# Kernel optimization log

Measured on AMD Instinct MI355X. Metric: run time of the kernel, lower is better.

Reference implementation:

```python
import jax, jax.numpy as jnp
import numpy as np

B = 4096      # batch of states
N = 32        # SVGD particles per state
D_ACT = 16    # action dim
D_OBS = 64    # obs dim
H = 256       # critic hidden width
STEPS = 3     # num_svgd_steps
LR = 0.1      # svgd_lr
LIMIT = 1.0   # act_limit


def q_mlp(obs, x, w1, b1, w2, b2, w3, b3):
    # SAC-style critic: q(obs, a) -> scalar per row. obs/x: [BN, *]
    h = jnp.concatenate([obs, x], axis=-1)
    h = jax.nn.relu(h @ w1 + b1)
    h = jax.nn.relu(h @ w2 + b2)
    return (h @ w3 + b3)[..., 0]  # [BN]


def rbf_kernel(X, Y):
    # X: [B, N, D] (differentiable), Y: [B, N, D] (detached copy of X)
    diff = X[:, :, None, :] - Y[:, None, :, :]          # [B, N, N, D]
    dist_sq = jnp.sum(diff * diff, axis=-1)             # [B, N, N]
    # median heuristic bandwidth per batch element
    med = jnp.median(dist_sq.reshape(dist_sq.shape[0], -1), axis=-1)
    h = med / np.log(N) + 1e-8
    gamma = jax.lax.stop_gradient(1.0 / (2.0 * h))      # [B]
    K = jnp.exp(-gamma[:, None, None] * dist_sq)        # [B, N, N]
    # dK/dX (grad wrt first argument)
    K_grad = -2.0 * gamma[:, None, None, None] * diff * K[..., None]  # [B,N,N,D]
    return K, diff, gamma, K_grad


def setup_inputs() -> dict:
    key = jax.random.key(0)
    ks = jax.random.split(key, 6)
    BN = B * N
    sc = lambda k, shp: jax.random.normal(k, shp, jnp.float32) * 0.05
    return {
        "obs": jax.random.normal(ks[0], (BN, D_OBS), jnp.float32),
        "a": jax.random.normal(ks[1], (BN, D_ACT), jnp.float32),
        "w1": sc(ks[2], (D_OBS + D_ACT, H)),
        "b1": jnp.zeros((H,), jnp.float32),
        "w2": sc(ks[3], (H, H)),
        "b2": jnp.zeros((H,), jnp.float32),
        "w3": sc(ks[4], (H, 1)),
        "b3": jnp.zeros((1,), jnp.float32),
    }


def reference(obs, a, w1, b1, w2, b2, w3, b3):
    # a0 arrives detached in the original (sampler(obs, a0.detach(), ...))
    a = jax.lax.stop_gradient(a)
    logp = jnp.zeros((B, N), jnp.float32)
    q_fn = lambda X: q_mlp(obs, X, w1, b1, w2, b2, w3, b3)
    q_vals = None
    for _ in range(STEPS):
        # log_prob = min(q1, q1) == q1; score = d(sum q)/dX via vjp
        q_vals, vjp_fn = jax.vjp(q_fn, a)                 # q_vals: [BN]
        score, = vjp_fn(jnp.ones_like(q_vals))            # [BN, D_ACT]
        X = a.reshape(B, N, D_ACT)
        S = score.reshape(B, N, D_ACT)
        K, diff, gamma, K_grad = rbf_kernel(X, jax.lax.stop_gradient(X))
        # phi = (K.detach() @ score - K_grad.sum(2)) / N
        drive = jnp.einsum('bij,bjd->bid', jax.lax.stop_gradient(K), S)
        phi = (drive - K_grad.sum(axis=2)) / N            # [B, N, D]
        # logp correction terms
        tmp1 = (K_grad * S[:, None, :, :]).sum(-1).mean(-1)                 # [B, N]
        tmp2 = -2.0 * gamma[:, None] * (((-K_grad) * diff).sum(-1)
                                        - D_ACT * K).mean(-1)               # [B, N]
        logp = logp - LR * (tmp1 + tmp2)
        # svgd_optim + clamp + detach
        a = a + LR * phi.reshape(B * N, D_ACT)
        a = jax.lax.stop_gradient(jnp.clip(a, -LIMIT, LIMIT))
    return a.reshape(B, N, D_ACT), logp, q_vals
```

## Files before the change

kernel.cpp:

```cpp
#include <hip/hip_runtime.h>
#include <hip/hip_bf16.h>
#include <math.h>

#define BNROWS (4096*32)
#define RB     64
#define LN32   3.4657359027997265f

typedef __attribute__((ext_vector_type(8))) short bf16x8;
typedef __attribute__((ext_vector_type(4))) float f32x4;

static __device__ __forceinline__ ushort f2bf(float x) {
    union { __hip_bfloat16 h; ushort u; } cv;
    cv.h = __float2bfloat16(x);
    return cv.u;
}

__global__ void obs_to_bf16(const float* __restrict__ obs,
                            ushort* __restrict__ obs_bf) {
    size_t i = ((size_t)blockIdx.x * 256 + threadIdx.x) * 4;
    float4 v = *(const float4*)&obs[i];
    ushort4 o;
    o.x = f2bf(v.x); o.y = f2bf(v.y); o.z = f2bf(v.z); o.w = f2bf(v.w);
    *(ushort4*)&obs_bf[i] = o;
}

__global__ void prep_pack(const float* __restrict__ w1,
                          const float* __restrict__ w2,
                          ushort* __restrict__ pB1, ushort* __restrict__ pB2,
                          ushort* __restrict__ pB3, ushort* __restrict__ pB4) {
    int g = blockIdx.x * 256 + threadIdx.x;
    ushort out[8];
    ushort* dst;
    if (g < 3072) {
        int lane = g & 63, gc = g >> 6;
        int t = gc / 3, c = gc % 3;
        int m = lane & 15, q = lane >> 4, n = t * 16 + m;
        #pragma unroll
        for (int j = 0; j < 8; ++j) {
            int k = c * 32 + q * 8 + j;
            out[j] = f2bf((k < 80) ? w1[k * 256 + n] : 0.f);
        }
        dst = &pB1[g * 8];
    } else if (g < 11264) {
        int gg = g - 3072;
        int lane = gg & 63, gc = gg >> 6;
        int t = gc >> 3, c = gc & 7;
        int m = lane & 15, q = lane >> 4, n = t * 16 + m;
        #pragma unroll
        for (int j = 0; j < 8; ++j)
            out[j] = f2bf(w2[(c * 32 + q * 8 + j) * 256 + n]);
        dst = &pB2[gg * 8];
    } else if (g < 19456) {
        int gg = g - 11264;
        int lane = gg & 63, gc = gg >> 6;
        int t = gc >> 3, c = gc & 7;
        int m = lane & 15, q = lane >> 4;
        #pragma unroll
        for (int j = 0; j < 8; ++j)
            out[j] = f2bf(w2[(t * 16 + m) * 256 + c * 32 + q * 8 + j]);
        dst = &pB3[gg * 8];
    } else if (g < 19968) {
        int gg = g - 19456;
        int lane = gg & 63, c = gg >> 6;
        int m = lane & 15, q = lane >> 4;
        #pragma unroll
        for (int j = 0; j < 8; ++j)
            out[j] = f2bf(w1[(64 + m) * 256 + c * 32 + q * 8 + j]);
        dst = &pB4[gg * 8];
    } else return;
    *(uint4*)dst = *(uint4*)out;
}

__global__ __launch_bounds__(512) void mlp_mfma(
    const ushort* __restrict__ obs_bf,
    const float* __restrict__ a_in,
    const float* __restrict__ b1,
    const float* __restrict__ b2,
    const float* __restrict__ w3,
    const float* __restrict__ b3,
    const ushort* __restrict__ pB1, const ushort* __restrict__ pB2,
    const ushort* __restrict__ pB3, const ushort* __restrict__ pB4,
    float* __restrict__ score,
    float* __restrict__ qout)
{
    __shared__ __align__(16) ushort B0[RB * 264];
    __shared__ __align__(16) ushort B1s[RB * 104];
    __shared__ float qpart[8][RB];
    __shared__ float bias1[256], bias2[256], w3s[256];

    const int tid  = threadIdx.x;
    const int row0 = blockIdx.x * RB;

    {
        int r = tid >> 3, ch = tid & 7;
        *(uint4*)&B1s[r * 104 + ch * 8] =
            *(const uint4*)&obs_bf[(size_t)(row0 + r) * 64 + ch * 8];
    }
    if (tid < 256) {
        int r = tid >> 2, d0 = (tid & 3) * 4;
        float4 av = *(const float4*)&a_in[(size_t)(row0 + r) * 16 + d0];
        ushort4 pv;
        pv.x = f2bf(av.x); pv.y = f2bf(av.y); pv.z = f2bf(av.z); pv.w = f2bf(av.w);
        *(ushort4*)&B1s[r * 104 + 64 + d0] = pv;
        ushort4 zv; zv.x = zv.y = zv.z = zv.w = 0;
        *(ushort4*)&B1s[r * 104 + 80 + d0] = zv;
        bias1[tid] = b1[tid]; bias2[tid] = b2[tid]; w3s[tid] = w3[tid];
    }
    __syncthreads();

    const int lane = tid & 63;
    const int w    = tid >> 6;
    const int m    = lane & 15;
    const int q    = lane >> 4;
    const int qk   = q * 8;

    f32x4 acc[4][2];
    unsigned relumask = 0u;

    #pragma unroll
    for (int tc = 0; tc < 2; ++tc)
        #pragma unroll
        for (int rt = 0; rt < 4; ++rt) acc[rt][tc] = (f32x4){0.f, 0.f, 0.f, 0.f};
    for (int c = 0; c < 3; ++c) {
        bf16x8 af[4];
        #pragma unroll
        for (int rt = 0; rt < 4; ++rt)
            af[rt] = *(const bf16x8*)&B1s[(rt * 16 + m) * 104 + c * 32 + qk];
        #pragma unroll
        for (int tc = 0; tc < 2; ++tc) {
            bf16x8 wfr = *(const bf16x8*)&pB1[(((w * 2 + tc) * 3 + c) * 64 + lane) * 8];
            #pragma unroll
            for (int rt = 0; rt < 4; ++rt)
                acc[rt][tc] = __builtin_amdgcn_mfma_f32_16x16x32_bf16(wfr, af[rt], acc[rt][tc], 0, 0, 0);
        }
    }
    #pragma unroll
    for (int tc = 0; tc < 2; ++tc) {
        const float4 bv = *(const float4*)&bias1[(w * 2 + tc) * 16 + q * 4];
        const float bva[4] = {bv.x, bv.y, bv.z, bv.w};
        #pragma unroll
        for (int rt = 0; rt < 4; ++rt) {
            ushort4 pk;
            float z0 = acc[rt][tc][0] + bva[0];
            float z1 = acc[rt][tc][1] + bva[1];
            float z2 = acc[rt][tc][2] + bva[2];
            float z3 = acc[rt][tc][3] + bva[3];
            if (z0 > 0.f) relumask |= 1u << (rt * 8 + tc * 4 + 0);
            if (z1 > 0.f) relumask |= 1u << (rt * 8 + tc * 4 + 1);
            if (z2 > 0.f) relumask |= 1u << (rt * 8 + tc * 4 + 2);
            if (z3 > 0.f) relumask |= 1u << (rt * 8 + tc * 4 + 3);
            pk.x = f2bf(fmaxf(z0, 0.f)); pk.y = f2bf(fmaxf(z1, 0.f));
            pk.z = f2bf(fmaxf(z2, 0.f)); pk.w = f2bf(fmaxf(z3, 0.f));
            *(ushort4*)&B0[(rt * 16 + m) * 264 + (w * 2 + tc) * 16 + q * 4] = pk;
        }
    }
    __syncthreads();

    #pragma unroll
    for (int tc = 0; tc < 2; ++tc)
        #pragma unroll
        for (int rt = 0; rt < 4; ++rt) acc[rt][tc] = (f32x4){0.f, 0.f, 0.f, 0.f};
    for (int c = 0; c < 8; ++c) {
        bf16x8 af[4];
        #pragma unroll
        for (int rt = 0; rt < 4; ++rt)
            af[rt] = *(const bf16x8*)&B0[(rt * 16 + m) * 264 + c * 32 + qk];
        #pragma unroll
        for (int tc = 0; tc < 2; ++tc) {
            bf16x8 wfr = *(const bf16x8*)&pB2[(((w * 2 + tc) * 8 + c) * 64 + lane) * 8];
            #pragma unroll
            for (int rt = 0; rt < 4; ++rt)
                acc[rt][tc] = __builtin_amdgcn_mfma_f32_16x16x32_bf16(wfr, af[rt], acc[rt][tc], 0, 0, 0);
        }
    }
    __syncthreads();
    {
        float qp[4] = {0.f, 0.f, 0.f, 0.f};
        #pragma unroll
        for (int tc = 0; tc < 2; ++tc) {
            const float4 bv = *(const float4*)&bias2[(w * 2 + tc) * 16 + q * 4];
            const float4 wv = *(const float4*)&w3s[(w * 2 + tc) * 16 + q * 4];
            const float bva[4] = {bv.x, bv.y, bv.z, bv.w};
            const float wva[4] = {wv.x, wv.y, wv.z, wv.w};
            #pragma unroll
            for (int rt = 0; rt < 4; ++rt) {
                ushort4 pk; float dz[4];
                #pragma unroll
                for (int i = 0; i < 4; ++i) {
                    float z = acc[rt][tc][i] + bva[i];
                    if (z > 0.f) { qp[rt] += z * wva[i]; dz[i] = wva[i]; }
                    else         { dz[i] = 0.f; }
                }
                pk.x = f2bf(dz[0]); pk.y = f2bf(dz[1]);
                pk.z = f2bf(dz[2]); pk.w = f2bf(dz[3]);
                *(ushort4*)&B0[(rt * 16 + m) * 264 + (w * 2 + tc) * 16 + q * 4] = pk;
            }
        }
        #pragma unroll
        for (int rt = 0; rt < 4; ++rt) {
            float v = qp[rt];
            v += __shfl_xor(v, 16); v += __shfl_xor(v, 32);
            if (q == 0) qpart[w][rt * 16 + m] = v;
        }
    }
    __syncthreads();

    if (tid < RB) {
        float qs = b3[0];
        #pragma unroll
        for (int ww = 0; ww < 8; ++ww) qs += qpart[ww][tid];
        qout[row0 + tid] = qs;
    }

    #pragma unroll
    for (int tc = 0; tc < 2; ++tc)
        #pragma unroll
        for (int rt = 0; rt < 4; ++rt) acc[rt][tc] = (f32x4){0.f, 0.f, 0.f, 0.f};
    for (int c = 0; c < 8; ++c) {
        bf16x8 af[4];
        #pragma unroll
        for (int rt = 0; rt < 4; ++rt)
            af[rt] = *(const bf16x8*)&B0[(rt * 16 + m) * 264 + c * 32 + qk];
        #pragma unroll
        for (int tc = 0; tc < 2; ++tc) {
            bf16x8 wfr = *(const bf16x8*)&pB3[(((w * 2 + tc) * 8 + c) * 64 + lane) * 8];
            #pragma unroll
            for (int rt = 0; rt < 4; ++rt)
                acc[rt][tc] = __builtin_amdgcn_mfma_f32_16x16x32_bf16(wfr, af[rt], acc[rt][tc], 0, 0, 0);
        }
    }
    __syncthreads();
    #pragma unroll
    for (int rt = 0; rt < 4; ++rt)
        #pragma unroll
        for (int tc = 0; tc < 2; ++tc) {
            ushort4 pk;
            pk.x = f2bf((relumask >> (rt * 8 + tc * 4 + 0)) & 1u ? acc[rt][tc][0] : 0.f);
            pk.y = f2bf((relumask >> (rt * 8 + tc * 4 + 1)) & 1u ? acc[rt][tc][1] : 0.f);
            pk.z = f2bf((relumask >> (rt * 8 + tc * 4 + 2)) & 1u ? acc[rt][tc][2] : 0.f);
            pk.w = f2bf((relumask >> (rt * 8 + tc * 4 + 3)) & 1u ? acc[rt][tc][3] : 0.f);
            *(ushort4*)&B0[(rt * 16 + m) * 264 + (w * 2 + tc) * 16 + q * 4] = pk;
        }
    __syncthreads();

    if (w < 4) {
        f32x4 acc2 = (f32x4){0.f, 0.f, 0.f, 0.f};
        for (int c = 0; c < 8; ++c) {
            bf16x8 af = *(const bf16x8*)&B0[(w * 16 + m) * 264 + c * 32 + qk];
            bf16x8 wfr = *(const bf16x8*)&pB4[(c * 64 + lane) * 8];
            acc2 = __builtin_amdgcn_mfma_f32_16x16x32_bf16(wfr, af, acc2, 0, 0, 0);
        }
        float4 o; o.x = acc2[0]; o.y = acc2[1]; o.z = acc2[2]; o.w = acc2[3];
        *(float4*)&score[(size_t)(row0 + w * 16 + m) * 16 + q * 4] = o;
    }
}

__global__ __launch_bounds__(256, 4) void svgd_kernel(
    const float* __restrict__ a_in,
    const float* __restrict__ score,
    const float* __restrict__ logp_in,
    float* __restrict__ logp_out,
    float* __restrict__ a_out,
    int first)
{
    __shared__ float X[32 * 17], S[32 * 17];
    __shared__ float KM[32 * 40];
    __shared__ int hist[2048];
    __shared__ int wsum[4];
    __shared__ int bbin, bexcl;
    __shared__ int redc[4];
    __shared__ unsigned redm[4];

    const int b = blockIdx.x, tid = threadIdx.x;
    const int lane = tid & 63, wv = tid >> 6;
    const size_t base = (size_t)b * 512;

    for (int idx = tid; idx < 512; idx += 256) {
        int r = idx >> 4, d = idx & 15;
        X[r * 17 + d] = a_in[base + idx];
        S[r * 17 + d] = score[base + idx];
    }
    __syncthreads();

    unsigned v[4]; float p[4];
    #pragma unroll
    for (int t = 0; t < 4; ++t) {
        int idx = tid + 256 * t, i = idx >> 5, j = idx & 31;
        float s = 0.f, pp = 0.f;
        #pragma unroll
        for (int d = 0; d < 16; ++d) {
            float df = X[i * 17 + d] - X[j * 17 + d];
            s  = fmaf(df, df, s);
            pp = fmaf(df, S[j * 17 + d], pp);
        }
        v[t] = __float_as_uint(s);
        p[t] = pp;
    }

    unsigned prefix = 0;
    int rank = 511;
    #pragma unroll
    for (int pass = 0; pass < 3; ++pass) {
        const int sh = (pass == 0) ? 21 : (pass == 1) ? 10 : 0;
        const unsigned dmask = (pass == 2) ? 1023u : 2047u;
        #pragma unroll
        for (int k = 0; k < 8; ++k) hist[tid + 256 * k] = 0;
        __syncthreads();
        #pragma unroll
        for (int t = 0; t < 4; ++t) {
            bool ok = (pass == 0) ||
                      ((v[t] >> (sh + ((pass == 1) ? 11 : 10))) == prefix);
            if (ok) atomicAdd(&hist[(v[t] >> sh) & dmask], 1);
        }
        __syncthreads();
        int c[8], ct = 0;
        #pragma unroll
        for (int k = 0; k < 8; ++k) { c[k] = hist[8 * tid + k]; ct += c[k]; }
        int inc = ct;
        #pragma unroll
        for (int off = 1; off < 64; off <<= 1) {
            int tt = __shfl_up(inc, off, 64);
            if (lane >= off) inc += tt;
        }
        if (lane == 63) wsum[wv] = inc;
        __syncthreads();
        int run = inc - ct;
        for (int ww = 0; ww < wv; ++ww) run += wsum[ww];
        #pragma unroll
        for (int k = 0; k < 8; ++k) {
            if (c[k] > 0 && rank >= run && rank < run + c[k]) {
                bbin = 8 * tid + k; bexcl = run;
            }
            run += c[k];
        }
        __syncthreads();
        prefix = (prefix << ((pass == 2) ? 10 : 11)) | (unsigned)bbin;
        rank -= bexcl;
    }
    const float v1 = __uint_as_float(prefix);

    float med;
    {
        int cle = 0;
        unsigned mgt = 0xFFFFFFFFu;
        #pragma unroll
        for (int t = 0; t < 4; ++t) {
            if (v[t] <= prefix) cle++;
            else mgt = min(mgt, v[t]);
        }
        #pragma unroll
        for (int off = 1; off < 64; off <<= 1) {
            cle += __shfl_xor(cle, off);
            mgt = min(mgt, (unsigned)__shfl_xor((int)mgt, off));
        }
        if (lane == 0) { redc[wv] = cle; redm[wv] = mgt; }
        __syncthreads();
        int C = redc[0] + redc[1] + redc[2] + redc[3];
        unsigned M = min(min(redm[0], redm[1]), min(redm[2], redm[3]));
        float v2 = (C >= 513) ? v1 : __uint_as_float(M);
        med = 0.5f * (v1 + v2);
    }
    const float gamma = 1.0f / (2.0f * (med / LN32 + 1e-8f));

    float kreg[4];
    #pragma unroll
    for (int t = 0; t < 4; ++t) {
        int idx = tid + 256 * t, i = idx >> 5, j = idx & 31;
        float kk = __expf(-gamma * __uint_as_float(v[t]));
        kreg[t] = kk;
        KM[i * 40 + j] = kk;
    }

    {
        float acc1[4], acc2[4];
        #pragma unroll
        for (int t = 0; t < 4; ++t) {
            float a1 = kreg[t] * p[t];
            float a2 = (2.f * gamma * __uint_as_float(v[t]) - 16.f) * kreg[t];
            #pragma unroll
            for (int off = 1; off < 32; off <<= 1) {
                a1 += __shfl_xor(a1, off);
                a2 += __shfl_xor(a2, off);
            }
            acc1[t] = a1; acc2[t] = a2;
        }
        if ((tid & 31) == 0) {
            #pragma unroll
            for (int t = 0; t < 4; ++t) {
                int i = (tid >> 5) + 8 * t;
                float tmp = -2.f * gamma * (acc1[t] + acc2[t]) * (1.f / 32.f);
                float prev = first ? 0.f : logp_in[b * 32 + i];
                logp_out[b * 32 + i] = prev - 0.1f * tmp;
            }
        }
    }
    __syncthreads();

    for (int idx = tid; idx < 512; idx += 256) {
        int i = idx >> 4, d = idx & 15;
        float s1 = 0.f, s2 = 0.f;
        float xi = X[i * 17 + d];
        #pragma unroll
        for (int j = 0; j < 32; ++j) {
            float kk = KM[i * 40 + j];
            s1 = fmaf(kk, S[j * 17 + d], s1);
            s2 = fmaf(kk, xi - X[j * 17 + d], s2);
        }
        float phi = (s1 + 2.f * gamma * s2) * (1.f / 32.f);
        float av = xi + 0.1f * phi;
        av = fminf(fmaxf(av, -1.f), 1.f);
        a_out[base + idx] = av;
    }
}

extern "C" void kernel_launch(void* const* d_in, const int* in_sizes, int n_in,
                              void* d_out, int out_size, void* d_ws, size_t ws_size,
                              hipStream_t stream) {
    const float* obs = (const float*)d_in[0];
    const float* a0  = (const float*)d_in[1];
    const float* w1  = (const float*)d_in[2];
    const float* b1  = (const float*)d_in[3];
    const float* w2  = (const float*)d_in[4];
    const float* b2  = (const float*)d_in[5];
    const float* w3  = (const float*)d_in[6];
    const float* b3  = (const float*)d_in[7];

    float* out_a    = (float*)d_out;
    float* out_logp = out_a + (size_t)BNROWS * 16;
    float* out_q    = out_logp + BNROWS;

    char* p = (char*)d_ws;
    ushort* pB1 = (ushort*)p; p += 24576 * 2;
    ushort* pB2 = (ushort*)p; p += 65536 * 2;
    ushort* pB3 = (ushort*)p; p += 65536 * 2;
    ushort* pB4 = (ushort*)p; p += 4096 * 2;
    ushort* obs_bf = (ushort*)p; p += (size_t)BNROWS * 64 * 2;
    float* abuf0 = (float*)p; p += (size_t)BNROWS * 16 * 4;
    float* abuf1 = (float*)p; p += (size_t)BNROWS * 16 * 4;
    float* scr   = (float*)p; p += (size_t)BNROWS * 16 * 4;
    float* logp  = (float*)p; p += (size_t)BNROWS * 4;
    float* qtmp  = (float*)p;

    prep_pack<<<78, 256, 0, stream>>>(w1, w2, pB1, pB2, pB3, pB4);
    obs_to_bf16<<<8192, 256, 0, stream>>>(obs, obs_bf);

    const int MB = BNROWS / RB;

    mlp_mfma<<<MB, 512, 0, stream>>>(obs_bf, a0, b1, b2, w3, b3,
                                     pB1, pB2, pB3, pB4, scr, qtmp);
    svgd_kernel<<<4096, 256, 0, stream>>>(a0, scr, nullptr, logp, abuf0, 1);
    mlp_mfma<<<MB, 512, 0, stream>>>(obs_bf, abuf0, b1, b2, w3, b3,
                                     pB1, pB2, pB3, pB4, scr, qtmp);
    svgd_kernel<<<4096, 256, 0, stream>>>(abuf0, scr, logp, logp, abuf1, 0);
    mlp_mfma<<<MB, 512, 0, stream>>>(obs_bf, abuf1, b1, b2, w3, b3,
                                     pB1, pB2, pB3, pB4, scr, out_q);
    svgd_kernel<<<4096, 256, 0, stream>>>(abuf1, scr, logp, out_logp, out_a, 0);
}
```

Measured before the change: 381.5 us.

## Process one SVGD state per wavefront, dropping block barriers in median select

The SVGD kernel now gives each 64-lane wavefront its own state (four states per block) rather than one state per 256-thread block. Syncthreads are removed, and the radix-select median switches from three 11-bit passes to four 8-bit passes on a 256-bin per-wave histogram, using ballot and shuffle. Loads are vectorized, the kernel matrix is stored with an XOR swizzle, and each lane accumulates eight output rows in registers. This aims to remove block-wide barrier and large-histogram costs. The price is higher register pressure from the 16-entry per-lane arrays and an extra select pass.

```diff
diff --git a/kernel.cpp b/kernel.cpp
--- a/kernel.cpp
+++ b/kernel.cpp
@@ -255,7 +255,7 @@
     }
 }
 
-__global__ __launch_bounds__(256, 4) void svgd_kernel(
+__global__ __launch_bounds__(256, 4) void svgd4(
     const float* __restrict__ a_in,
     const float* __restrict__ score,
     const float* __restrict__ logp_in,
@@ -263,153 +263,179 @@
     float* __restrict__ a_out,
     int first)
 {
-    __shared__ float X[32 * 17], S[32 * 17];
-    __shared__ float KM[32 * 40];
-    __shared__ int hist[2048];
-    __shared__ int wsum[4];
-    __shared__ int bbin, bexcl;
-    __shared__ int redc[4];
-    __shared__ unsigned redm[4];
-
-    const int b = blockIdx.x, tid = threadIdx.x;
-    const int lane = tid & 63, wv = tid >> 6;
-    const size_t base = (size_t)b * 512;
-
-    for (int idx = tid; idx < 512; idx += 256) {
-        int r = idx >> 4, d = idx & 15;
-        X[r * 17 + d] = a_in[base + idx];
-        S[r * 17 + d] = score[base + idx];
-    }
-    __syncthreads();
-
-    unsigned v[4]; float p[4];
-    #pragma unroll
-    for (int t = 0; t < 4; ++t) {
-        int idx = tid + 256 * t, i = idx >> 5, j = idx & 31;
-        float s = 0.f, pp = 0.f;
-        #pragma unroll
-        for (int d = 0; d < 16; ++d) {
-            float df = X[i * 17 + d] - X[j * 17 + d];
-            s  = fmaf(df, df, s);
-            pp = fmaf(df, S[j * 17 + d], pp);
-        }
-        v[t] = __float_as_uint(s);
+    __shared__ __align__(16) float X4[4][32 * 20];
+    __shared__ __align__(16) float S4[4][32 * 20];
+    __shared__ __align__(16) float KM4[4][1024];
+
+    const int tid    = threadIdx.x;
+    const int wv     = tid >> 6;
+    const int lane   = tid & 63;
+    const int stateg = blockIdx.x * 4 + wv;
+    const size_t base = (size_t)stateg * 512;
+
+    float* X  = X4[wv];
+    float* S  = S4[wv];
+    float* KM = KM4[wv];
+    int*   h  = (int*)KM4[wv];
+
+    {
+        int g0 = lane * 8;
+        int r = g0 >> 4, d0 = g0 & 15;
+        float4 va0 = *(const float4*)&a_in[base + g0];
+        float4 va1 = *(const float4*)&a_in[base + g0 + 4];
+        float4 vs0 = *(const float4*)&score[base + g0];
+        float4 vs1 = *(const float4*)&score[base + g0 + 4];
+        *(float4*)&X[r * 20 + d0]     = va0;
+        *(float4*)&X[r * 20 + d0 + 4] = va1;
+        *(float4*)&S[r * 20 + d0]     = vs0;
+        *(float4*)&S[r * 20 + d0 + 4] = vs1;
+    }
+    __asm__ volatile("s_waitcnt lgkmcnt(0)" ::: "memory");
+
+    const int half = lane >> 5;
+    const int j    = lane & 31;
+
+    float Xj[16], Sj[16];
+    #pragma unroll
+    for (int d0 = 0; d0 < 16; d0 += 4) {
+        float4 xv = *(const float4*)&X[j * 20 + d0];
+        float4 sv = *(const float4*)&S[j * 20 + d0];
+        Xj[d0 + 0] = xv.x; Xj[d0 + 1] = xv.y; Xj[d0 + 2] = xv.z; Xj[d0 + 3] = xv.w;
+        Sj[d0 + 0] = sv.x; Sj[d0 + 1] = sv.y; Sj[d0 + 2] = sv.z; Sj[d0 + 3] = sv.w;
+    }
+
+    unsigned v[16]; float p[16];
+    #pragma unroll
+    for (int t = 0; t < 16; ++t) {
+        const float* Xi = &X[(half * 16 + t) * 20];
+        float ss = 0.f, pp = 0.f;
+        #pragma unroll
+        for (int d0 = 0; d0 < 16; d0 += 4) {
+            float4 xv = *(const float4*)&Xi[d0];
+            float df0 = xv.x - Xj[d0 + 0];
+            float df1 = xv.y - Xj[d0 + 1];
+            float df2 = xv.z - Xj[d0 + 2];
+            float df3 = xv.w - Xj[d0 + 3];
+            ss = fmaf(df0, df0, ss); pp = fmaf(df0, Sj[d0 + 0], pp);
+            ss = fmaf(df1, df1, ss); pp = fmaf(df1, Sj[d0 + 1], pp);
+            ss = fmaf(df2, df2, ss); pp = fmaf(df2, Sj[d0 + 2], pp);
+            ss = fmaf(df3, df3, ss); pp = fmaf(df3, Sj[d0 + 3], pp);
+        }
+        v[t] = __float_as_uint(ss);
         p[t] = pp;
     }
 
     unsigned prefix = 0;
     int rank = 511;
-    #pragma unroll
-    for (int pass = 0; pass < 3; ++pass) {
-        const int sh = (pass == 0) ? 21 : (pass == 1) ? 10 : 0;
-        const unsigned dmask = (pass == 2) ? 1023u : 2047u;
-        #pragma unroll
-        for (int k = 0; k < 8; ++k) hist[tid + 256 * k] = 0;
-        __syncthreads();
-        #pragma unroll
-        for (int t = 0; t < 4; ++t) {
-            bool ok = (pass == 0) ||
-                      ((v[t] >> (sh + ((pass == 1) ? 11 : 10))) == prefix);
-            if (ok) atomicAdd(&hist[(v[t] >> sh) & dmask], 1);
-        }
-        __syncthreads();
-        int c[8], ct = 0;
-        #pragma unroll
-        for (int k = 0; k < 8; ++k) { c[k] = hist[8 * tid + k]; ct += c[k]; }
+    #pragma unroll 1
+    for (int pass = 0; pass < 4; ++pass) {
+        const int sh = 24 - pass * 8;
+        int4 z4; z4.x = z4.y = z4.z = z4.w = 0;
+        *(int4*)&h[lane * 4] = z4;
+        __asm__ volatile("s_waitcnt lgkmcnt(0)" ::: "memory");
+        #pragma unroll
+        for (int t = 0; t < 16; ++t) {
+            bool ok = (pass == 0) || ((v[t] >> (sh + 8)) == prefix);
+            if (ok) atomicAdd(&h[(v[t] >> sh) & 255], 1);
+        }
+        __asm__ volatile("s_waitcnt lgkmcnt(0)" ::: "memory");
+        int4 c4 = *(const int4*)&h[lane * 4];
+        int c[4] = {c4.x, c4.y, c4.z, c4.w};
+        int ct = c[0] + c[1] + c[2] + c[3];
         int inc = ct;
         #pragma unroll
         for (int off = 1; off < 64; off <<= 1) {
             int tt = __shfl_up(inc, off, 64);
             if (lane >= off) inc += tt;
         }
-        if (lane == 63) wsum[wv] = inc;
-        __syncthreads();
         int run = inc - ct;
-        for (int ww = 0; ww < wv; ++ww) run += wsum[ww];
-        #pragma unroll
-        for (int k = 0; k < 8; ++k) {
-            if (c[k] > 0 && rank >= run && rank < run + c[k]) {
-                bbin = 8 * tid + k; bexcl = run;
+        int binf = -1, runf = 0;
+        #pragma unroll
+        for (int e = 0; e < 4; ++e) {
+            if (binf < 0 && rank >= run && rank < run + c[e]) {
+                binf = lane * 4 + e; runf = run;
             }
-            run += c[k];
-        }
-        __syncthreads();
-        prefix = (prefix << ((pass == 2) ? 10 : 11)) | (unsigned)bbin;
-        rank -= bexcl;
+            run += c[e];
+        }
+        unsigned long long bm = __ballot(binf >= 0);
+        int src = __ffsll(bm) - 1;
+        int bin  = __shfl(binf, src);
+        int excl = __shfl(runf, src);
+        prefix = (prefix << 8) | (unsigned)bin;
+        rank -= excl;
     }
     const float v1 = __uint_as_float(prefix);
 
-    float med;
-    {
-        int cle = 0;
-        unsigned mgt = 0xFFFFFFFFu;
-        #pragma unroll
-        for (int t = 0; t < 4; ++t) {
-            if (v[t] <= prefix) cle++;
-            else mgt = min(mgt, v[t]);
-        }
-        #pragma unroll
-        for (int off = 1; off < 64; off <<= 1) {
-            cle += __shfl_xor(cle, off);
-            mgt = min(mgt, (unsigned)__shfl_xor((int)mgt, off));
-        }
-        if (lane == 0) { redc[wv] = cle; redm[wv] = mgt; }
-        __syncthreads();
-        int C = redc[0] + redc[1] + redc[2] + redc[3];
-        unsigned M = min(min(redm[0], redm[1]), min(redm[2], redm[3]));
-        float v2 = (C >= 513) ? v1 : __uint_as_float(M);
-        med = 0.5f * (v1 + v2);
-    }
+    int cle = 0;
+    unsigned mgt = 0xFFFFFFFFu;
+    #pragma unroll
+    for (int t = 0; t < 16; ++t) {
+        if (v[t] <= prefix) cle++;
+        else mgt = min(mgt, v[t]);
+    }
+    #pragma unroll
+    for (int off = 1; off < 64; off <<= 1) {
+        cle += __shfl_xor(cle, off);
+        mgt = min(mgt, (unsigned)__shfl_xor((int)mgt, off));
+    }
+    const float v2  = (cle >= 513) ? v1 : __uint_as_float(mgt);
+    const float med = 0.5f * (v1 + v2);
     const float gamma = 1.0f / (2.0f * (med / LN32 + 1e-8f));
 
-    float kreg[4];
-    #pragma unroll
-    for (int t = 0; t < 4; ++t) {
-        int idx = tid + 256 * t, i = idx >> 5, j = idx & 31;
+    float kreg[16];
+    #pragma unroll
+    for (int t = 0; t < 16; ++t) {
+        int i = half * 16 + t;
         float kk = __expf(-gamma * __uint_as_float(v[t]));
         kreg[t] = kk;
-        KM[i * 40 + j] = kk;
-    }
+        KM[i * 32 + (j ^ i)] = kk;
+    }
+
+    #pragma unroll
+    for (int t = 0; t < 16; ++t) {
+        float a1 = kreg[t] * p[t];
+        float a2 = fmaf(2.f * gamma, __uint_as_float(v[t]), -16.f) * kreg[t];
+        float acc = a1 + a2;
+        #pragma unroll
+        for (int off = 1; off < 32; off <<= 1)
+            acc += __shfl_xor(acc, off);
+        if (j == 0) {
+            int row = half * 16 + t;
+            float tmp = -2.f * gamma * acc * (1.f / 32.f);
+            float prev = first ? 0.f : logp_in[stateg * 32 + row];
+            logp_out[stateg * 32 + row] = prev - 0.1f * tmp;
+        }
+    }
+    __asm__ volatile("s_waitcnt lgkmcnt(0)" ::: "memory");
 
     {
-        float acc1[4], acc2[4];
-        #pragma unroll
-        for (int t = 0; t < 4; ++t) {
-            float a1 = kreg[t] * p[t];
-            float a2 = (2.f * gamma * __uint_as_float(v[t]) - 16.f) * kreg[t];
+        const int d  = lane & 15;
+        const int i0 = lane >> 4;
+        float s1[8], s2[8], xi[8];
+        #pragma unroll
+        for (int e = 0; e < 8; ++e) {
+            s1[e] = 0.f; s2[e] = 0.f;
+            xi[e] = X[(i0 + 4 * e) * 20 + d];
+        }
+        for (int jj = 0; jj < 32; ++jj) {
+            float xjv = X[jj * 20 + d];
+            float sjv = S[jj * 20 + d];
             #pragma unroll
-            for (int off = 1; off < 32; off <<= 1) {
-                a1 += __shfl_xor(a1, off);
-                a2 += __shfl_xor(a2, off);
+            for (int e = 0; e < 8; ++e) {
+                int i = i0 + 4 * e;
+                float kk = KM[i * 32 + (jj ^ i)];
+                s1[e] = fmaf(kk, sjv, s1[e]);
+                s2[e] = fmaf(kk, xi[e] - xjv, s2[e]);
             }
-            acc1[t] = a1; acc2[t] = a2;
-        }
-        if ((tid & 31) == 0) {
-            #pragma unroll
-            for (int t = 0; t < 4; ++t) {
-                int i = (tid >> 5) + 8 * t;
-                float tmp = -2.f * gamma * (acc1[t] + acc2[t]) * (1.f / 32.f);
-                float prev = first ? 0.f : logp_in[b * 32 + i];
-                logp_out[b * 32 + i] = prev - 0.1f * tmp;
-            }
-        }
-    }
-    __syncthreads();
-
-    for (int idx = tid; idx < 512; idx += 256) {
-        int i = idx >> 4, d = idx & 15;
-        float s1 = 0.f, s2 = 0.f;
-        float xi = X[i * 17 + d];
-        #pragma unroll
-        for (int j = 0; j < 32; ++j) {
-            float kk = KM[i * 40 + j];
-            s1 = fmaf(kk, S[j * 17 + d], s1);
-            s2 = fmaf(kk, xi - X[j * 17 + d], s2);
-        }
-        float phi = (s1 + 2.f * gamma * s2) * (1.f / 32.f);
-        float av = xi + 0.1f * phi;
-        av = fminf(fmaxf(av, -1.f), 1.f);
-        a_out[base + idx] = av;
+        }
+        #pragma unroll
+        for (int e = 0; e < 8; ++e) {
+            int i = i0 + 4 * e;
+            float phi = (s1[e] + 2.f * gamma * s2[e]) * (1.f / 32.f);
+            float av = xi[e] + 0.1f * phi;
+            av = fminf(fmaxf(av, -1.f), 1.f);
+            a_out[base + i * 16 + d] = av;
+        }
     }
 }
 
@@ -445,14 +471,15 @@
     obs_to_bf16<<<8192, 256, 0, stream>>>(obs, obs_bf);
 
     const int MB = BNROWS / RB;
+    const int SB = 4096 / 4;
 
     mlp_mfma<<<MB, 512, 0, stream>>>(obs_bf, a0, b1, b2, w3, b3,
                                      pB1, pB2, pB3, pB4, scr, qtmp);
-    svgd_kernel<<<4096, 256, 0, stream>>>(a0, scr, nullptr, logp, abuf0, 1);
+    svgd4<<<SB, 256, 0, stream>>>(a0, scr, nullptr, logp, abuf0, 1);
     mlp_mfma<<<MB, 512, 0, stream>>>(obs_bf, abuf0, b1, b2, w3, b3,
                                      pB1, pB2, pB3, pB4, scr, qtmp);
-    svgd_kernel<<<4096, 256, 0, stream>>>(abuf0, scr, logp, logp, abuf1, 0);
+    svgd4<<<SB, 256, 0, stream>>>(abuf0, scr, logp, logp, abuf1, 0);
     mlp_mfma<<<MB, 512, 0, stream>>>(obs_bf, abuf1, b1, b2, w3, b3,
                                      pB1, pB2, pB3, pB4, scr, out_q);
-    svgd_kernel<<<4096, 256, 0, stream>>>(abuf1, scr, logp, out_logp, out_a, 0);
-}
+    svgd4<<<SB, 256, 0, stream>>>(abuf1, scr, logp, out_logp, out_a, 0);
+}
```

Measured after the change: 775.0 us. 103% more time.
